# Performance work log

Hardware: AMD Instinct MI355X
Metric: run time of the kernel (lower is better)

Reference implementation:

```python
import jax, jax.numpy as jnp
import numpy as np

TAU = 0.1
SELF_MASK = 1e6  # added to diagonal of self-distances (y_neg is x)


def _cdist(a, b):
    # pairwise L2 distances, [Na, Nb]; eps keeps sqrt grad finite at 0
    sq = (a * a).sum(-1)[:, None] + (b * b).sum(-1)[None, :] - 2.0 * (a @ b.T)
    return jnp.sqrt(jnp.maximum(sq, 1e-12))


def setup_inputs() -> dict:
    key = jax.random.key(0)
    k1, k2 = jax.random.split(key)
    N, D = 4096, 512
    return {
        "x": jax.random.normal(k1, (N, D), dtype=jnp.float32),
        "y_pos": jax.random.normal(k2, (N, D), dtype=jnp.float32),
    }


def reference(x, y_pos):
    # compute_drift_velocity with y_neg = x (training/loss path)
    N = x.shape[0]
    dist_pos = _cdist(x, y_pos)                      # [N, N]
    dist_neg = _cdist(x, x) + SELF_MASK * jnp.eye(N, dtype=x.dtype)
    logits = -jnp.concatenate([dist_pos, dist_neg], axis=1) / TAU  # [N, 2N]
    # dual normalization: row softmax * column softmax, geometric mean
    A_row = jax.nn.softmax(logits, axis=-1)
    A_col = jax.nn.softmax(logits, axis=0)
    A = jnp.sqrt(A_row * A_col)
    A_pos, A_neg = A[:, :N], A[:, N:]
    drift = A_pos @ y_pos - A_neg @ x                # [N, D]
    return drift
```

## Files before the change

### kernel.cpp

```cpp
#include <hip/hip_runtime.h>
#include <math.h>

#define NN   4096
#define DD   512
#define TWON 8192

typedef _Float16 half_t;
typedef unsigned short u16;
using half8  = __attribute__((ext_vector_type(8))) half_t;
using short8 = __attribute__((ext_vector_type(8))) short;
using f32x4  = __attribute__((ext_vector_type(4))) float;

__device__ __forceinline__ u16 f2bf(float f) {
    unsigned u = __float_as_uint(f);
    u += 0x7fffu + ((u >> 16) & 1u);
    return (u16)(u >> 16);
}
__device__ __forceinline__ float bf2f(u16 h) {
    return __uint_as_float(((unsigned)h) << 16);
}
__device__ __forceinline__ void gl16(const void* g, void* l) {
    __builtin_amdgcn_global_load_lds(
        (const __attribute__((address_space(1))) void*)g,
        (__attribute__((address_space(3))) void*)l, 16, 0, 0);
}
__device__ __forceinline__ f32x4 mfma16h(half8 a, half8 b, f32x4 c) {
    return __builtin_amdgcn_mfma_f32_16x16x32_f16(a, b, c, 0, 0, 0);
}
__device__ __forceinline__ f32x4 mfma16b(short8 a, short8 b, f32x4 c) {
    return __builtin_amdgcn_mfma_f32_16x16x32_bf16(a, b, c, 0, 0, 0);
}

__global__ __launch_bounds__(64)
void prep_k(const float* __restrict__ x, const float* __restrict__ y,
            half_t* __restrict__ bhi, float* __restrict__ nb) {
    int r = blockIdx.x;
    int l = threadIdx.x;
    const float* src = (r < NN) ? (y + (size_t)r * DD) : (x + (size_t)(r - NN) * DD);
    float4 v0 = *reinterpret_cast<const float4*>(src + l * 8);
    float4 v1 = *reinterpret_cast<const float4*>(src + l * 8 + 4);
    float e[8] = {v0.x, v0.y, v0.z, v0.w, v1.x, v1.y, v1.z, v1.w};
    float s = 0.f;
    half8 h;
    #pragma unroll
    for (int q = 0; q < 8; ++q) {
        s += e[q] * e[q];
        h[q] = (half_t)e[q];
    }
    *reinterpret_cast<half8*>(bhi + (size_t)r * DD + l * 8) = h;
    #pragma unroll
    for (int off = 32; off; off >>= 1) s += __shfl_down(s, off);
    if (l == 0) nb[r] = s;
}

__global__ __launch_bounds__(256)
void b2tr_k(const half_t* __restrict__ bhi, u16* __restrict__ b2t) {
    __shared__ half_t tl[32][33];
    int k0 = blockIdx.x * 32, d0 = blockIdx.y * 32;
    int tx = threadIdx.x, ty = threadIdx.y;
    #pragma unroll
    for (int j = 0; j < 4; ++j)
        tl[ty + 8 * j][tx] = bhi[(size_t)(k0 + ty + 8 * j) * DD + d0 + tx];
    __syncthreads();
    float sgn = (k0 < NN) ? 1.f : -1.f;
    #pragma unroll
    for (int j = 0; j < 4; ++j) {
        float v = (float)tl[tx][ty + 8 * j] * sgn;
        b2t[(size_t)(d0 + ty + 8 * j) * TWON + k0 + tx] = f2bf(v);
    }
}

__global__ __launch_bounds__(256)
void gemm1_k(const half_t* __restrict__ bhi,
             const float* __restrict__ nb, u16* __restrict__ Ef,
             float* __restrict__ Ct,
             float* __restrict__ rpm, float* __restrict__ rps,
             float* __restrict__ cpm, float* __restrict__ cps) {
    __shared__ unsigned char lds[32768];
    const int t = threadIdx.x;
    const int wave = t >> 6, lane = t & 63;
    const int i0 = blockIdx.y * 128, j0 = blockIdx.x * 128;
    const int wm = (wave >> 1) * 64, wn = (wave & 1) * 64;
    const half_t* ahig = bhi + (size_t)NN * DD;
    f32x4 acc[4][4] = {};
    for (int k0 = 0; k0 < DD; k0 += 64) {
        __syncthreads();
        #pragma unroll
        for (int q = 0; q < 4; ++q) {
            const int dbase = (wave * 4 + q) * 1024;
            const int p  = dbase + lane * 16;
            const int r  = p >> 7;
            const int cb = (p & 127) ^ ((r & 7) << 4);
            const size_t offA = (size_t)(i0 + r) * DD + k0 + (cb >> 1);
            const size_t offB = (size_t)(j0 + r) * DD + k0 + (cb >> 1);
            gl16(ahig + offA, lds + dbase);
            gl16(bhi  + offB, lds + 16384 + dbase);
        }
        asm volatile("s_waitcnt vmcnt(0)" ::: "memory");
        __builtin_amdgcn_sched_barrier(0);
        __syncthreads();
        #pragma unroll
        for (int kk = 0; kk < 2; ++kk) {
            half8 ah[4];
            #pragma unroll
            for (int m = 0; m < 4; ++m) {
                const int row = wm + m * 16 + (lane & 15);
                const int off = row * 128 + ((kk * 64 + (lane >> 4) * 16) ^ ((row & 7) << 4));
                ah[m] = *reinterpret_cast<const half8*>(lds + off);
            }
            #pragma unroll
            for (int n = 0; n < 4; ++n) {
                const int row = wn + n * 16 + (lane & 15);
                const int off = row * 128 + ((kk * 64 + (lane >> 4) * 16) ^ ((row & 7) << 4));
                half8 bh = *reinterpret_cast<const half8*>(lds + 16384 + off);
                #pragma unroll
                for (int m = 0; m < 4; ++m)
                    acc[m][n] = mfma16h(ah[m], bh, acc[m][n]);
            }
        }
    }
    float nbj[4];
    #pragma unroll
    for (int n = 0; n < 4; ++n) nbj[n] = nb[j0 + wn + n * 16 + (lane & 15)];
    float tmax = -3.0e38f;
    #pragma unroll
    for (int m = 0; m < 4; ++m) {
        #pragma unroll
        for (int r4 = 0; r4 < 4; ++r4) {
            const int i = i0 + wm + m * 16 + (lane >> 4) * 4 + r4;
            const float nxi = nb[NN + i];
            #pragma unroll
            for (int n = 0; n < 4; ++n) {
                const int j = j0 + wn + n * 16 + (lane & 15);
                float sq = nxi + nbj[n] - 2.0f * acc[m][n][r4];
                float lg = -10.0f * sqrtf(fmaxf(sq, 1e-12f));
                if (j == i + NN) lg = -1e7f;
                acc[m][n][r4] = lg;
                tmax = fmaxf(tmax, lg);
            }
        }
    }
    #pragma unroll
    for (int off = 1; off < 64; off <<= 1) tmax = fmaxf(tmax, __shfl_xor(tmax, off));
    __syncthreads();
    float* red = reinterpret_cast<float*>(lds);
    if (lane == 0) red[wave] = tmax;
    __syncthreads();
    const float C = fmaxf(fmaxf(red[0], red[1]), fmaxf(red[2], red[3]));
    __syncthreads();
    if (t == 0) Ct[blockIdx.y * 64 + blockIdx.x] = C;
    float rs[16] = {}, cs[4] = {};
    #pragma unroll
    for (int m = 0; m < 4; ++m)
        #pragma unroll
        for (int r4 = 0; r4 < 4; ++r4) {
            const int idx = m * 4 + r4;
            const int i = i0 + wm + m * 16 + (lane >> 4) * 4 + r4;
            #pragma unroll
            for (int n = 0; n < 4; ++n) {
                const int j = j0 + wn + n * 16 + (lane & 15);
                float e = __expf(acc[m][n][r4] - C);
                Ef[(size_t)i * TWON + j] = f2bf(e);
                rs[idx] += e;
                cs[n]   += e;
            }
        }
    #pragma unroll
    for (int off = 1; off < 16; off <<= 1) {
        #pragma unroll
        for (int idx = 0; idx < 16; ++idx) rs[idx] += __shfl_xor(rs[idx], off);
    }
    #pragma unroll
    for (int off = 16; off < 64; off <<= 1) {
        #pragma unroll
        for (int n = 0; n < 4; ++n) cs[n] += __shfl_xor(cs[n], off);
    }
    if ((lane & 15) == 0) {
        #pragma unroll
        for (int m = 0; m < 4; ++m)
            #pragma unroll
            for (int r4 = 0; r4 < 4; ++r4) {
                const int r = wm + m * 16 + (lane >> 4) * 4 + r4;
                red[(wave & 1) * 128 + r] = rs[m * 4 + r4];
            }
    }
    if (lane < 16) {
        #pragma unroll
        for (int n = 0; n < 4; ++n) {
            const int c = wn + n * 16 + lane;
            red[256 + (wave >> 1) * 128 + c] = cs[n];
        }
    }
    __syncthreads();
    if (t < 128) {
        float S = red[t] + red[128 + t];
        rpm[(size_t)blockIdx.x * NN + i0 + t] = C;
        rps[(size_t)blockIdx.x * NN + i0 + t] = S;
    } else {
        const int c = t - 128;
        float S = red[256 + c] + red[384 + c];
        cpm[(size_t)blockIdx.y * TWON + j0 + c] = C;
        cps[(size_t)blockIdx.y * TWON + j0 + c] = S;
    }
}

__global__ __launch_bounds__(256)
void row_comb_k(const float* __restrict__ rpm, const float* __restrict__ rps,
                float* __restrict__ rm, float* __restrict__ rrs) {
    int i = blockIdx.x * 256 + threadIdx.x;
    float M = -3.0e38f;
    for (int tt = 0; tt < TWON / 128; ++tt) M = fmaxf(M, rpm[(size_t)tt * NN + i]);
    float S = 0.f;
    for (int tt = 0; tt < TWON / 128; ++tt)
        S += rps[(size_t)tt * NN + i] * __expf(rpm[(size_t)tt * NN + i] - M);
    rm[i] = M; rrs[i] = rsqrtf(S);
}

__global__ __launch_bounds__(256)
void col_comb_k(const float* __restrict__ cpm, const float* __restrict__ cps,
                float* __restrict__ Pj) {
    int j = blockIdx.x * 256 + threadIdx.x;
    float M = -3.0e38f;
    for (int tt = 0; tt < NN / 128; ++tt) M = fmaxf(M, cpm[(size_t)tt * TWON + j]);
    float S = 0.f;
    for (int tt = 0; tt < NN / 128; ++tt)
        S += cps[(size_t)tt * TWON + j] * __expf(cpm[(size_t)tt * TWON + j] - M);
    Pj[j] = -0.5f * M - 0.5f * logf(S);
}

__global__ __launch_bounds__(512, 4)
void gemm2_k(const u16* __restrict__ Ef, const u16* __restrict__ b2t,
             const float* __restrict__ Ct, const float* __restrict__ rm,
             const float* __restrict__ Pj, const float* __restrict__ rrs,
             unsigned* __restrict__ part) {
    __shared__ unsigned char lds[32768];
    const int t = threadIdx.x;
    const int wave = t >> 6, lane = t & 63;
    const int sw = blockIdx.x;
    const int kslice = sw & 7;
    const int idx2 = sw >> 3;
    const int db = idx2 & 3;
    const int iblk = idx2 >> 2;
    const int i0 = iblk * 128;
    const int d0 = db * 128;
    const int kbase = kslice * 1024;
    const int mh = wave >> 2, dq = wave & 3;
    const int sr = t >> 2;
    const int kc = (t & 3) * 16;
    const int aw0 = sr * 128 + ((kc * 2) ^ ((sr & 7) << 4));
    const int aw1 = sr * 128 + (((kc + 8) * 2) ^ ((sr & 7) << 4));
    const float rmh = 0.5f * rm[i0 + sr];
    const int NT = 16;
    f32x4 acc[4][2] = {};
    for (int it = 0; it < NT; ++it) {
        __syncthreads();
        #pragma unroll
        for (int q = 0; q < 2; ++q) {
            const int dbase = (wave * 2 + q) * 1024;
            const int p  = dbase + lane * 16;
            const int r  = p >> 7;
            const int cb = (p & 127) ^ ((r & 7) << 4);
            gl16(b2t + (size_t)(d0 + r) * TWON + kbase + it * 64 + (cb >> 1),
                 lds + 16384 + dbase);
        }
        {
            const int k = kbase + it * 64 + kc;
            const u16* ep = Ef + (size_t)(i0 + sr) * TWON + k;
            short8 aE0 = *reinterpret_cast<const short8*>(ep);
            short8 aE1 = *reinterpret_cast<const short8*>(ep + 8);
            float4 p0 = *reinterpret_cast<const float4*>(Pj + k);
            float4 p1 = *reinterpret_cast<const float4*>(Pj + k + 4);
            float4 p2 = *reinterpret_cast<const float4*>(Pj + k + 8);
            float4 p3 = *reinterpret_cast<const float4*>(Pj + k + 12);
            const float arg = Ct[iblk * 64 + ((kbase + it * 64) >> 7)] - rmh;
            short8 g0, g1;
            g0[0] = (short)f2bf(bf2f((u16)aE0[0]) * __expf(arg + p0.x));
            g0[1] = (short)f2bf(bf2f((u16)aE0[1]) * __expf(arg + p0.y));
            g0[2] = (short)f2bf(bf2f((u16)aE0[2]) * __expf(arg + p0.z));
            g0[3] = (short)f2bf(bf2f((u16)aE0[3]) * __expf(arg + p0.w));
            g0[4] = (short)f2bf(bf2f((u16)aE0[4]) * __expf(arg + p1.x));
            g0[5] = (short)f2bf(bf2f((u16)aE0[5]) * __expf(arg + p1.y));
            g0[6] = (short)f2bf(bf2f((u16)aE0[6]) * __expf(arg + p1.z));
            g0[7] = (short)f2bf(bf2f((u16)aE0[7]) * __expf(arg + p1.w));
            g1[0] = (short)f2bf(bf2f((u16)aE1[0]) * __expf(arg + p2.x));
            g1[1] = (short)f2bf(bf2f((u16)aE1[1]) * __expf(arg + p2.y));
            g1[2] = (short)f2bf(bf2f((u16)aE1[2]) * __expf(arg + p2.z));
            g1[3] = (short)f2bf(bf2f((u16)aE1[3]) * __expf(arg + p2.w));
            g1[4] = (short)f2bf(bf2f((u16)aE1[4]) * __expf(arg + p3.x));
            g1[5] = (short)f2bf(bf2f((u16)aE1[5]) * __expf(arg + p3.y));
            g1[6] = (short)f2bf(bf2f((u16)aE1[6]) * __expf(arg + p3.z));
            g1[7] = (short)f2bf(bf2f((u16)aE1[7]) * __expf(arg + p3.w));
            *reinterpret_cast<short8*>(lds + aw0) = g0;
            *reinterpret_cast<short8*>(lds + aw1) = g1;
        }
        asm volatile("s_waitcnt vmcnt(0)" ::: "memory");
        __builtin_amdgcn_sched_barrier(0);
        __syncthreads();
        #pragma unroll
        for (int kk = 0; kk < 2; ++kk) {
            short8 af[4], bfr[2];
            #pragma unroll
            for (int m = 0; m < 4; ++m) {
                const int row = mh * 64 + m * 16 + (lane & 15);
                const int off = row * 128 +
                                ((kk * 64 + (lane >> 4) * 16) ^ ((row & 7) << 4));
                af[m] = *reinterpret_cast<const short8*>(lds + off);
            }
            #pragma unroll
            for (int n = 0; n < 2; ++n) {
                const int row = dq * 32 + n * 16 + (lane & 15);
                const int off = 16384 + row * 128 +
                                ((kk * 64 + (lane >> 4) * 16) ^ ((row & 7) << 4));
                bfr[n] = *reinterpret_cast<const short8*>(lds + off);
            }
            #pragma unroll
            for (int m = 0; m < 4; ++m)
                #pragma unroll
                for (int n = 0; n < 2; ++n)
                    acc[m][n] = mfma16b(af[m], bfr[n], acc[m][n]);
        }
    }
    unsigned* pout = part + ((size_t)(kslice * 128 + idx2) * 512 + t) * 16;
    #pragma unroll
    for (int m = 0; m < 4; ++m) {
        float rf[4];
        #pragma unroll
        for (int r4 = 0; r4 < 4; ++r4)
            rf[r4] = rrs[i0 + mh * 64 + m * 16 + (lane >> 4) * 4 + r4];
        unsigned pk[4];
        #pragma unroll
        for (int n = 0; n < 2; ++n) {
            pk[n * 2]     = (unsigned)f2bf(acc[m][n][0] * rf[0]) |
                            ((unsigned)f2bf(acc[m][n][1] * rf[1]) << 16);
            pk[n * 2 + 1] = (unsigned)f2bf(acc[m][n][2] * rf[2]) |
                            ((unsigned)f2bf(acc[m][n][3] * rf[3]) << 16);
        }
        *reinterpret_cast<uint4*>(pout + m * 4) = *reinterpret_cast<uint4*>(pk);
    }
}

__global__ __launch_bounds__(512)
void reduce_k(const unsigned* __restrict__ part, float* __restrict__ out) {
    const int b = blockIdx.x;
    const int mq = b & 3, pos = b >> 2;
    const int db = pos & 3, iblk = pos >> 2;
    const int t = threadIdx.x;
    const int lane = t & 63, wave = t >> 6;
    const int mh = wave >> 2, dq = wave & 3;
    float s[8] = {};
    #pragma unroll
    for (int ks = 0; ks < 8; ++ks) {
        const unsigned* p = part + ((size_t)(ks * 128 + pos) * 512 + t) * 16 + mq * 4;
        uint4 a = *reinterpret_cast<const uint4*>(p);
        unsigned u[4] = {a.x, a.y, a.z, a.w};
        #pragma unroll
        for (int n = 0; n < 2; ++n) {
            s[n * 4 + 0] += bf2f((u16)(u[n * 2] & 0xffffu));
            s[n * 4 + 1] += bf2f((u16)(u[n * 2] >> 16));
            s[n * 4 + 2] += bf2f((u16)(u[n * 2 + 1] & 0xffffu));
            s[n * 4 + 3] += bf2f((u16)(u[n * 2 + 1] >> 16));
        }
    }
    #pragma unroll
    for (int n = 0; n < 2; ++n)
        #pragma unroll
        for (int r4 = 0; r4 < 4; ++r4) {
            const int i = iblk * 128 + mh * 64 + mq * 16 + (lane >> 4) * 4 + r4;
            const int d = db * 128 + dq * 32 + n * 16 + (lane & 15);
            out[(size_t)i * DD + d] = s[n * 4 + r4];
        }
}

extern "C" void kernel_launch(void* const* d_in, const int* in_sizes, int n_in,
                              void* d_out, int out_size, void* d_ws, size_t ws_size,
                              hipStream_t stream) {
    const float* x = (const float*)d_in[0];
    const float* y = (const float*)d_in[1];
    float* out = (float*)d_out;

    char* w = (char*)d_ws;
    const size_t OFF_EF   = 0;
    const size_t OFF_BHI  = 67108864;
    const size_t OFF_B2T  = OFF_BHI + 8388608;
    const size_t OFF_PART = OFF_B2T + 8388608;
    const size_t OFF_RPM  = OFF_PART + 67108864;
    const size_t OFF_RPS  = OFF_RPM + 1048576;
    const size_t OFF_CPM  = OFF_RPS + 1048576;
    const size_t OFF_CPS  = OFF_CPM + 1048576;
    const size_t OFF_CT   = OFF_CPS + 1048576;
    const size_t OFF_TAIL = OFF_CT + 65536;

    u16*      Ef   = (u16*)(w + OFF_EF);
    half_t*   bhi  = (half_t*)(w + OFF_BHI);
    u16*      b2t  = (u16*)(w + OFF_B2T);
    unsigned* part = (unsigned*)(w + OFF_PART);
    float*    rpm  = (float*)(w + OFF_RPM);
    float*    rps  = (float*)(w + OFF_RPS);
    float*    cpm  = (float*)(w + OFF_CPM);
    float*    cps  = (float*)(w + OFF_CPS);
    float*    Ct   = (float*)(w + OFF_CT);
    float*    nb   = (float*)(w + OFF_TAIL);
    float*    rm   = nb  + TWON;
    float*    rrs  = rm  + NN;
    float*    Pj   = rrs + NN;

    prep_k<<<TWON, 64, 0, stream>>>(x, y, bhi, nb);
    gemm1_k<<<dim3(TWON / 128, NN / 128), 256, 0, stream>>>(bhi, nb, Ef, Ct,
                                                            rpm, rps, cpm, cps);
    row_comb_k<<<NN / 256, 256, 0, stream>>>(rpm, rps, rm, rrs);
    col_comb_k<<<TWON / 256, 256, 0, stream>>>(cpm, cps, Pj);
    b2tr_k<<<dim3(TWON / 32, DD / 32), dim3(32, 8), 0, stream>>>(bhi, b2t);
    gemm2_k<<<1024, 512, 0, stream>>>(Ef, b2t, Ct, rm, Pj, rrs, part);
    reduce_k<<<512, 512, 0, stream>>>(part, out);
}
```

Measured before the change: 187.4 us.

## Transpose gemm1 MFMA output for packed Ef stores, use exp2 domain, fuse comb kernels

Swaps the MFMA operand order in gemm1 so each lane holds four consecutive columns. Ef is then written as packed 8-byte stores instead of scattered 2-byte stores, and the row/column partial-sum reductions are reorganised to match. Logits are scaled by log2(e) so the exponentials use hardware exp2/log2/sqrt intrinsics, and bf16 conversion switches to truncation instead of round-to-nearest. The row and column combine kernels are merged into one launch. The risk is a slight loss of accuracy from truncation and the approximate intrinsics.

```diff
diff --git a/kernel.cpp b/kernel.cpp
--- a/kernel.cpp
+++ b/kernel.cpp
@@ -10,6 +10,12 @@
 using half8  = __attribute__((ext_vector_type(8))) half_t;
 using short8 = __attribute__((ext_vector_type(8))) short;
 using f32x4  = __attribute__((ext_vector_type(4))) float;
+
+#define NLOG2E_10 (-14.4269504089f)
+
+__device__ __forceinline__ float exp2_f(float x) { return __builtin_amdgcn_exp2f(x); }
+__device__ __forceinline__ float log2_f(float x) { return __builtin_amdgcn_logf(x); }
+__device__ __forceinline__ float sqrt_f(float x) { return __builtin_amdgcn_sqrtf(x); }
 
 __device__ __forceinline__ u16 f2bf(float f) {
     unsigned u = __float_as_uint(f);
@@ -115,26 +121,31 @@
                 half8 bh = *reinterpret_cast<const half8*>(lds + 16384 + off);
                 #pragma unroll
                 for (int m = 0; m < 4; ++m)
-                    acc[m][n] = mfma16h(ah[m], bh, acc[m][n]);
+                    acc[m][n] = mfma16h(bh, ah[m], acc[m][n]);
             }
         }
     }
-    float nbj[4];
-    #pragma unroll
-    for (int n = 0; n < 4; ++n) nbj[n] = nb[j0 + wn + n * 16 + (lane & 15)];
+    float nxi[4];
+    #pragma unroll
+    for (int m = 0; m < 4; ++m) nxi[m] = nb[NN + i0 + wm + m * 16 + (lane & 15)];
+    float4 nbj4[4];
+    #pragma unroll
+    for (int n = 0; n < 4; ++n)
+        nbj4[n] = *reinterpret_cast<const float4*>(nb + j0 + wn + n * 16 + (lane >> 4) * 4);
     float tmax = -3.0e38f;
     #pragma unroll
     for (int m = 0; m < 4; ++m) {
-        #pragma unroll
-        for (int r4 = 0; r4 < 4; ++r4) {
-            const int i = i0 + wm + m * 16 + (lane >> 4) * 4 + r4;
-            const float nxi = nb[NN + i];
-            #pragma unroll
-            for (int n = 0; n < 4; ++n) {
-                const int j = j0 + wn + n * 16 + (lane & 15);
-                float sq = nxi + nbj[n] - 2.0f * acc[m][n][r4];
-                float lg = -10.0f * sqrtf(fmaxf(sq, 1e-12f));
-                if (j == i + NN) lg = -1e7f;
+        const int irel = i0 + wm + m * 16 + (lane & 15) + NN - j0;
+        #pragma unroll
+        for (int n = 0; n < 4; ++n) {
+            #pragma unroll
+            for (int r4 = 0; r4 < 4; ++r4) {
+                const int jrel = wn + n * 16 + (lane >> 4) * 4 + r4;
+                float nbj = (r4 == 0) ? nbj4[n].x : (r4 == 1) ? nbj4[n].y
+                          : (r4 == 2) ? nbj4[n].z : nbj4[n].w;
+                float sq = nxi[m] + nbj - 2.0f * acc[m][n][r4];
+                float lg = NLOG2E_10 * sqrt_f(fmaxf(sq, 1e-12f));
+                if (jrel == irel) lg = -1e7f;
                 acc[m][n][r4] = lg;
                 tmax = fmaxf(tmax, lg);
             }
@@ -149,47 +160,48 @@
     const float C = fmaxf(fmaxf(red[0], red[1]), fmaxf(red[2], red[3]));
     __syncthreads();
     if (t == 0) Ct[blockIdx.y * 64 + blockIdx.x] = C;
-    float rs[16] = {}, cs[4] = {};
-    #pragma unroll
-    for (int m = 0; m < 4; ++m)
-        #pragma unroll
-        for (int r4 = 0; r4 < 4; ++r4) {
-            const int idx = m * 4 + r4;
-            const int i = i0 + wm + m * 16 + (lane >> 4) * 4 + r4;
-            #pragma unroll
-            for (int n = 0; n < 4; ++n) {
-                const int j = j0 + wn + n * 16 + (lane & 15);
-                float e = __expf(acc[m][n][r4] - C);
-                Ef[(size_t)i * TWON + j] = f2bf(e);
-                rs[idx] += e;
-                cs[n]   += e;
-            }
-        }
+    float rs[4] = {}, cs[16] = {};
+    #pragma unroll
+    for (int m = 0; m < 4; ++m) {
+        const size_t ibase = (size_t)(i0 + wm + m * 16 + (lane & 15)) * TWON;
+        #pragma unroll
+        for (int n = 0; n < 4; ++n) {
+            float e0 = exp2_f(acc[m][n][0] - C);
+            float e1 = exp2_f(acc[m][n][1] - C);
+            float e2 = exp2_f(acc[m][n][2] - C);
+            float e3 = exp2_f(acc[m][n][3] - C);
+            uint2 pk;
+            pk.x = (__float_as_uint(e0) >> 16) | (__float_as_uint(e1) & 0xffff0000u);
+            pk.y = (__float_as_uint(e2) >> 16) | (__float_as_uint(e3) & 0xffff0000u);
+            const int j = j0 + wn + n * 16 + (lane >> 4) * 4;
+            *reinterpret_cast<uint2*>(Ef + ibase + j) = pk;
+            rs[m] += e0 + e1 + e2 + e3;
+            cs[n * 4 + 0] += e0; cs[n * 4 + 1] += e1;
+            cs[n * 4 + 2] += e2; cs[n * 4 + 3] += e3;
+        }
+    }
+    #pragma unroll
+    for (int off = 16; off < 64; off <<= 1) {
+        #pragma unroll
+        for (int m = 0; m < 4; ++m) rs[m] += __shfl_xor(rs[m], off);
+    }
     #pragma unroll
     for (int off = 1; off < 16; off <<= 1) {
         #pragma unroll
-        for (int idx = 0; idx < 16; ++idx) rs[idx] += __shfl_xor(rs[idx], off);
-    }
-    #pragma unroll
-    for (int off = 16; off < 64; off <<= 1) {
-        #pragma unroll
-        for (int n = 0; n < 4; ++n) cs[n] += __shfl_xor(cs[n], off);
+        for (int q = 0; q < 16; ++q) cs[q] += __shfl_xor(cs[q], off);
+    }
+    if (lane < 16) {
+        #pragma unroll
+        for (int m = 0; m < 4; ++m)
+            red[(wave & 1) * 128 + wm + m * 16 + lane] = rs[m];
     }
     if ((lane & 15) == 0) {
         #pragma unroll
-        for (int m = 0; m < 4; ++m)
-            #pragma unroll
-            for (int r4 = 0; r4 < 4; ++r4) {
-                const int r = wm + m * 16 + (lane >> 4) * 4 + r4;
-                red[(wave & 1) * 128 + r] = rs[m * 4 + r4];
-            }
-    }
-    if (lane < 16) {
-        #pragma unroll
-        for (int n = 0; n < 4; ++n) {
-            const int c = wn + n * 16 + lane;
-            red[256 + (wave >> 1) * 128 + c] = cs[n];
-        }
+        for (int n = 0; n < 4; ++n)
+            #pragma unroll
+            for (int r4 = 0; r4 < 4; ++r4)
+                red[256 + (wave >> 1) * 128 + (wave & 1) * 64 + n * 16 + (lane >> 4) * 4 + r4]
+                    = cs[n * 4 + r4];
     }
     __syncthreads();
     if (t < 128) {
@@ -205,27 +217,27 @@
 }
 
 __global__ __launch_bounds__(256)
-void row_comb_k(const float* __restrict__ rpm, const float* __restrict__ rps,
-                float* __restrict__ rm, float* __restrict__ rrs) {
-    int i = blockIdx.x * 256 + threadIdx.x;
-    float M = -3.0e38f;
-    for (int tt = 0; tt < TWON / 128; ++tt) M = fmaxf(M, rpm[(size_t)tt * NN + i]);
-    float S = 0.f;
-    for (int tt = 0; tt < TWON / 128; ++tt)
-        S += rps[(size_t)tt * NN + i] * __expf(rpm[(size_t)tt * NN + i] - M);
-    rm[i] = M; rrs[i] = rsqrtf(S);
-}
-
-__global__ __launch_bounds__(256)
-void col_comb_k(const float* __restrict__ cpm, const float* __restrict__ cps,
-                float* __restrict__ Pj) {
-    int j = blockIdx.x * 256 + threadIdx.x;
-    float M = -3.0e38f;
-    for (int tt = 0; tt < NN / 128; ++tt) M = fmaxf(M, cpm[(size_t)tt * TWON + j]);
-    float S = 0.f;
-    for (int tt = 0; tt < NN / 128; ++tt)
-        S += cps[(size_t)tt * TWON + j] * __expf(cpm[(size_t)tt * TWON + j] - M);
-    Pj[j] = -0.5f * M - 0.5f * logf(S);
+void comb_k(const float* __restrict__ rpm, const float* __restrict__ rps,
+            const float* __restrict__ cpm, const float* __restrict__ cps,
+            float* __restrict__ rm, float* __restrict__ rrs, float* __restrict__ Pj) {
+    const int b = blockIdx.x;
+    if (b < 16) {
+        int i = b * 256 + threadIdx.x;
+        float M = -3.0e38f;
+        for (int tt = 0; tt < TWON / 128; ++tt) M = fmaxf(M, rpm[(size_t)tt * NN + i]);
+        float S = 0.f;
+        for (int tt = 0; tt < TWON / 128; ++tt)
+            S += rps[(size_t)tt * NN + i] * exp2_f(rpm[(size_t)tt * NN + i] - M);
+        rm[i] = M; rrs[i] = rsqrtf(S);
+    } else {
+        int j = (b - 16) * 256 + threadIdx.x;
+        float M = -3.0e38f;
+        for (int tt = 0; tt < NN / 128; ++tt) M = fmaxf(M, cpm[(size_t)tt * TWON + j]);
+        float S = 0.f;
+        for (int tt = 0; tt < NN / 128; ++tt)
+            S += cps[(size_t)tt * TWON + j] * exp2_f(cpm[(size_t)tt * TWON + j] - M);
+        Pj[j] = -0.5f * M - 0.5f * log2_f(S);
+    }
 }
 
 __global__ __launch_bounds__(512, 4)
@@ -274,22 +286,22 @@
             float4 p3 = *reinterpret_cast<const float4*>(Pj + k + 12);
             const float arg = Ct[iblk * 64 + ((kbase + it * 64) >> 7)] - rmh;
             short8 g0, g1;
-            g0[0] = (short)f2bf(bf2f((u16)aE0[0]) * __expf(arg + p0.x));
-            g0[1] = (short)f2bf(bf2f((u16)aE0[1]) * __expf(arg + p0.y));
-            g0[2] = (short)f2bf(bf2f((u16)aE0[2]) * __expf(arg + p0.z));
-            g0[3] = (short)f2bf(bf2f((u16)aE0[3]) * __expf(arg + p0.w));
-            g0[4] = (short)f2bf(bf2f((u16)aE0[4]) * __expf(arg + p1.x));
-            g0[5] = (short)f2bf(bf2f((u16)aE0[5]) * __expf(arg + p1.y));
-            g0[6] = (short)f2bf(bf2f((u16)aE0[6]) * __expf(arg + p1.z));
-            g0[7] = (short)f2bf(bf2f((u16)aE0[7]) * __expf(arg + p1.w));
-            g1[0] = (short)f2bf(bf2f((u16)aE1[0]) * __expf(arg + p2.x));
-            g1[1] = (short)f2bf(bf2f((u16)aE1[1]) * __expf(arg + p2.y));
-            g1[2] = (short)f2bf(bf2f((u16)aE1[2]) * __expf(arg + p2.z));
-            g1[3] = (short)f2bf(bf2f((u16)aE1[3]) * __expf(arg + p2.w));
-            g1[4] = (short)f2bf(bf2f((u16)aE1[4]) * __expf(arg + p3.x));
-            g1[5] = (short)f2bf(bf2f((u16)aE1[5]) * __expf(arg + p3.y));
-            g1[6] = (short)f2bf(bf2f((u16)aE1[6]) * __expf(arg + p3.z));
-            g1[7] = (short)f2bf(bf2f((u16)aE1[7]) * __expf(arg + p3.w));
+            g0[0] = (short)(__float_as_uint(bf2f((u16)aE0[0]) * exp2_f(arg + p0.x)) >> 16);
+            g0[1] = (short)(__float_as_uint(bf2f((u16)aE0[1]) * exp2_f(arg + p0.y)) >> 16);
+            g0[2] = (short)(__float_as_uint(bf2f((u16)aE0[2]) * exp2_f(arg + p0.z)) >> 16);
+            g0[3] = (short)(__float_as_uint(bf2f((u16)aE0[3]) * exp2_f(arg + p0.w)) >> 16);
+            g0[4] = (short)(__float_as_uint(bf2f((u16)aE0[4]) * exp2_f(arg + p1.x)) >> 16);
+            g0[5] = (short)(__float_as_uint(bf2f((u16)aE0[5]) * exp2_f(arg + p1.y)) >> 16);
+            g0[6] = (short)(__float_as_uint(bf2f((u16)aE0[6]) * exp2_f(arg + p1.z)) >> 16);
+            g0[7] = (short)(__float_as_uint(bf2f((u16)aE0[7]) * exp2_f(arg + p1.w)) >> 16);
+            g1[0] = (short)(__float_as_uint(bf2f((u16)aE1[0]) * exp2_f(arg + p2.x)) >> 16);
+            g1[1] = (short)(__float_as_uint(bf2f((u16)aE1[1]) * exp2_f(arg + p2.y)) >> 16);
+            g1[2] = (short)(__float_as_uint(bf2f((u16)aE1[2]) * exp2_f(arg + p2.z)) >> 16);
+            g1[3] = (short)(__float_as_uint(bf2f((u16)aE1[3]) * exp2_f(arg + p2.w)) >> 16);
+            g1[4] = (short)(__float_as_uint(bf2f((u16)aE1[4]) * exp2_f(arg + p3.x)) >> 16);
+            g1[5] = (short)(__float_as_uint(bf2f((u16)aE1[5]) * exp2_f(arg + p3.y)) >> 16);
+            g1[6] = (short)(__float_as_uint(bf2f((u16)aE1[6]) * exp2_f(arg + p3.z)) >> 16);
+            g1[7] = (short)(__float_as_uint(bf2f((u16)aE1[7]) * exp2_f(arg + p3.w)) >> 16);
             *reinterpret_cast<short8*>(lds + aw0) = g0;
             *reinterpret_cast<short8*>(lds + aw1) = g1;
         }
@@ -407,8 +419,7 @@
     prep_k<<<TWON, 64, 0, stream>>>(x, y, bhi, nb);
     gemm1_k<<<dim3(TWON / 128, NN / 128), 256, 0, stream>>>(bhi, nb, Ef, Ct,
                                                             rpm, rps, cpm, cps);
-    row_comb_k<<<NN / 256, 256, 0, stream>>>(rpm, rps, rm, rrs);
-    col_comb_k<<<TWON / 256, 256, 0, stream>>>(cpm, cps, Pj);
+    comb_k<<<48, 256, 0, stream>>>(rpm, rps, cpm, cps, rm, rrs, Pj);
     b2tr_k<<<dim3(TWON / 32, DD / 32), dim3(32, 8), 0, stream>>>(bhi, b2t);
     gemm2_k<<<1024, 512, 0, stream>>>(Ef, b2t, Ct, rm, Pj, rrs, part);
     reduce_k<<<512, 512, 0, stream>>>(part, out);
```

Result: faster. 175.5 us (-6.4%).
